# Kernel tuning notes

Hardware: AMD Instinct MI355X
Metric: run time of the kernel (lower is better)

Reference implementation:

```python
import jax, jax.numpy as jnp
import numpy as np

HEAD_NUM = 16
PAD = 0.0
MASKS_FUTURE = True


def setup_inputs() -> dict:
    key = jax.random.key(0)
    ks = jax.random.split(key, 7)
    B, S, D = 2, 2048, 1024
    scale = 0.02
    return {
        "q": jax.random.normal(ks[0], (B, S, D), dtype=jnp.float32),
        "k": jax.random.normal(ks[1], (B, S, D), dtype=jnp.float32),
        "v": jax.random.normal(ks[2], (B, S, D), dtype=jnp.float32),
        "w_q": jax.random.normal(ks[3], (D, D), dtype=jnp.float32) * scale,
        "w_k": jax.random.normal(ks[4], (D, D), dtype=jnp.float32) * scale,
        "w_v": jax.random.normal(ks[5], (D, D), dtype=jnp.float32) * scale,
        "w_o": jax.random.normal(ks[6], (D, D), dtype=jnp.float32) * scale,
    }


def _split_head(x):
    # [B, S, D] -> [B, H, S, D/H]
    B, S, D = x.shape
    return x.reshape(B, S, HEAD_NUM, D // HEAD_NUM).transpose(0, 2, 1, 3)


def reference(q, k, v, w_q, w_k, w_v, w_o):
    qp = _split_head(q @ w_q)  # [B, H, Sq, dk]
    kp = _split_head(k @ w_k)  # [B, H, Sk, dk]
    vp = _split_head(v @ w_v)  # [B, H, Sk, dv]
    d_k = qp.shape[-1]
    scores = jnp.einsum("bhqd,bhkd->bhqk", qp, kp) / jnp.sqrt(jnp.float32(d_k))
    # mask where scores equal PAD (faithful to tf.equal(head_qk, PAD))
    mask = scores == PAD
    if MASKS_FUTURE:
        # tf.linalg.band_part(mask, -1, 0): keep lower triangle, zero elsewhere
        Sq, Sk = scores.shape[-2], scores.shape[-1]
        tril = jnp.tril(jnp.ones((Sq, Sk), dtype=bool))
        mask = mask & tril
    neg = jnp.finfo(jnp.float32).min
    scores = jnp.where(mask, neg, scores)
    attn = jax.nn.softmax(scores, axis=-1)
    # keep_prob = 1.0 -> dropout is identity
    attn = jnp.where(mask, PAD, attn)
    out = jnp.einsum("bhqk,bhkd->bhqd", attn, vp)  # [B, H, Sq, dv/H]
    B, H, S, dh = out.shape
    concat = out.transpose(0, 2, 1, 3).reshape(B, S, H * dh)
    return concat @ w_o
```

## Files before the change

kernel.cpp:

```cpp
#include <hip/hip_runtime.h>
#include <hip/hip_bf16.h>

typedef unsigned short u16;
typedef unsigned int u32;
typedef short short8 __attribute__((ext_vector_type(8)));
typedef float float4v __attribute__((ext_vector_type(4)));
typedef u32 u32x2 __attribute__((ext_vector_type(2)));

#define SEQ 2048
#define DIM 1024
#define NHEAD 16
#define MROWS 4096
#define NE ((size_t)MROWS * DIM)
#define WN ((size_t)DIM * DIM)

#if __has_builtin(__builtin_amdgcn_exp2f)
#define EXP2(x) __builtin_amdgcn_exp2f(x)
#else
#define EXP2(x) exp2f(x)
#endif

__device__ inline u16 f2bf(float f) {
    union { float f; unsigned u; } v; v.f = f;
    unsigned r = v.u + 0x7fffu + ((v.u >> 16) & 1u);
    return (u16)(r >> 16);
}
__device__ inline float bf2f(u16 s) {
    union { unsigned u; float f; } v; v.u = ((unsigned)s) << 16;
    return v.f;
}
__device__ inline u32 pk2bf(float a, float b) {
    union { __hip_bfloat162 h; u32 u; } cv;
    cv.h = __float22bfloat162_rn(float2{a, b});
    return cv.u;
}
__device__ inline void gld16(const void* g, void* l) {
    __builtin_amdgcn_global_load_lds(
        (const __attribute__((address_space(1))) void*)g,
        (__attribute__((address_space(3))) void*)l, 16, 0, 0);
}

__global__ __launch_bounds__(256) void convert_qkv(
    const float* __restrict__ q, const float* __restrict__ k,
    const float* __restrict__ v, u16* __restrict__ dst)
{
    const int z = blockIdx.y;
    const float* s = (z == 0) ? q : (z == 1) ? k : v;
    const size_t i = ((size_t)blockIdx.x * 256 + threadIdx.x) * 8;
    float4v a = *(const float4v*)(s + i);
    float4v b = *(const float4v*)(s + i + 4);
    short8 o;
    for (int e = 0; e < 4; e++) { o[e] = (short)f2bf(a[e]); o[4 + e] = (short)f2bf(b[e]); }
    *(short8*)(dst + z * NE + i) = o;
}

__global__ __launch_bounds__(256) void transpose_w(
    const float* __restrict__ w0, const float* __restrict__ w1,
    const float* __restrict__ w2, const float* __restrict__ w3,
    u16* __restrict__ Wt)
{
    __shared__ u16 T[64 * 66];
    const int z = blockIdx.z;
    const float* src = (z == 0) ? w0 : (z == 1) ? w1 : (z == 2) ? w2 : w3;
    const int kt = blockIdx.x * 64, nt = blockIdx.y * 64;
    const int tid = threadIdx.x;

    {
        const int row = tid >> 2, cg = (tid & 3) * 16;
        const float* sp = src + (size_t)(kt + row) * DIM + nt + cg;
        for (int i4 = 0; i4 < 4; i4++) {
            float4v f = *(const float4v*)(sp + i4 * 4);
            for (int e = 0; e < 4; e++)
                T[row * 66 + cg + i4 * 4 + e] = f2bf(f[e]);
        }
    }
    __syncthreads();
    {
        const int nr = tid >> 2, kg = (tid & 3) * 16;
        u16* dp = Wt + (size_t)z * WN + (size_t)(nt + nr) * DIM + kt + kg;
        short8 o0, o1;
        for (int e = 0; e < 8; e++) {
            o0[e] = (short)T[(kg + e) * 66 + nr];
            o1[e] = (short)T[(kg + 8 + e) * 66 + nr];
        }
        *(short8*)(dp) = o0;
        *(short8*)(dp + 8) = o1;
    }
}

__global__ __launch_bounds__(256) void transpose_v(
    const u16* __restrict__ Vn, u16* __restrict__ Vt)
{
    __shared__ u16 T[64 * 72];
    const int bh = blockIdx.x, s0 = blockIdx.y * 64;
    const int b = bh >> 4, h = bh & 15;
    const int tid = threadIdx.x;
    for (int cc = 0; cc < 2; cc++) {
        int c = tid + cc * 256;
        const u16* src = Vn + (size_t)(b * SEQ + s0 + (c >> 3)) * DIM + h * 64 + (c & 7) * 8;
        *(short8*)&T[(c >> 3) * 72 + (c & 7) * 8] = *(const short8*)src;
    }
    __syncthreads();
    for (int cc = 0; cc < 2; cc++) {
        int c = tid + cc * 256;
        int d = c >> 3, sc_ = c & 7;
        short8 o;
        for (int e = 0; e < 8; e++) o[e] = (short)T[(sc_ * 8 + e) * 72 + d];
        *(short8*)(Vt + ((size_t)bh * 64 + d) * SEQ + s0 + sc_ * 8) = o;
    }
}

template <typename OT>
__device__ __forceinline__ void gemm_body(
    const u16* __restrict__ A, const u16* __restrict__ W, OT* __restrict__ C)
{
    __shared__ u16 Alds[128 * 32];
    __shared__ u16 Wlds[128 * 32];

    const int tid = threadIdx.x;
    const int lane = tid & 63;
    const int quad = lane >> 4, l16 = lane & 15;
    const int wave = tid >> 6, wr = wave >> 1, wc = wave & 1;
    const int m0 = blockIdx.x * 128, n0 = blockIdx.y * 128;

    float4v acc[4][4];
    float4v vz = {0.f, 0.f, 0.f, 0.f};
    for (int i = 0; i < 4; i++)
        for (int j = 0; j < 4; j++) acc[i][j] = vz;

    const int c0 = tid, c1 = 256 + tid;
    const u16* a0 = A + (size_t)(m0 + (c0 >> 2)) * DIM + (c0 & 3) * 8;
    const u16* a1 = A + (size_t)(m0 + (c1 >> 2)) * DIM + (c1 & 3) * 8;
    const u16* w0 = W + (size_t)(n0 + (c0 >> 2)) * DIM + (c0 & 3) * 8;
    const u16* w1 = W + (size_t)(n0 + (c1 >> 2)) * DIM + (c1 & 3) * 8;

    for (int k0 = 0; k0 < DIM; k0 += 32) {
        gld16(a0 + k0, &Alds[c0 * 8]);
        gld16(a1 + k0, &Alds[c1 * 8]);
        gld16(w0 + k0, &Wlds[c0 * 8]);
        gld16(w1 + k0, &Wlds[c1 * 8]);
        __syncthreads();

        short8 a[4], b[4];
        for (int i = 0; i < 4; i++)
            a[i] = *(const short8*)&Alds[(wr * 64 + i * 16 + l16) * 32 + quad * 8];
        for (int j = 0; j < 4; j++)
            b[j] = *(const short8*)&Wlds[(wc * 64 + j * 16 + l16) * 32 + quad * 8];
        for (int i = 0; i < 4; i++)
            for (int j = 0; j < 4; j++)
                acc[i][j] = __builtin_amdgcn_mfma_f32_16x16x32_bf16(a[i], b[j], acc[i][j], 0, 0, 0);
        __syncthreads();
    }

    for (int i = 0; i < 4; i++) {
        int row = m0 + wr * 64 + i * 16 + quad * 4;
        for (int j = 0; j < 4; j++) {
            int col = n0 + wc * 64 + j * 16 + l16;
            for (int r = 0; r < 4; r++) {
                if constexpr (__is_same(OT, float))
                    C[(size_t)(row + r) * DIM + col] = acc[i][j][r];
                else
                    C[(size_t)(row + r) * DIM + col] = f2bf(acc[i][j][r]);
            }
        }
    }
}

__global__ __launch_bounds__(256) void gemm_qkv(
    const u16* __restrict__ Abf, const u16* __restrict__ Wt, u16* __restrict__ QKVb)
{
    const int z = blockIdx.z;
    gemm_body<u16>(Abf + (size_t)z * NE, Wt + (size_t)(z + 1) * WN, QKVb + (size_t)z * NE);
}
__global__ __launch_bounds__(256) void gemm_out(
    const u16* __restrict__ Cb, const u16* __restrict__ Wt, float* __restrict__ out)
{
    gemm_body<float>(Cb, Wt, out);
}

__global__ __launch_bounds__(256) void attn_kernel(
    const u16* __restrict__ Q, const u16* __restrict__ K,
    const u16* __restrict__ Vtg, u16* __restrict__ O)
{
    __shared__ u16 Klds[128 * 64];
    __shared__ u16 Vt[64 * 128];
    __shared__ u16 Pl[4][64 * 40];
    __shared__ float Llds[4][64];
    float* bufA = (float*)Klds;
    float* bufB = (float*)Vt;

    const int bh = blockIdx.x;
    const int q0 = blockIdx.y * 64;
    const int tid = threadIdx.x;
    const int lane = tid & 63, w = tid >> 6;
    const int quad = lane >> 4, l16 = lane & 15;

    const size_t base = (size_t)(bh >> 4) * SEQ * DIM + (bh & 15) * 64;
    const u16* Qp = Q + base;
    const u16* Kp = K + base;
    u16* Op = O + base;
    const u16* Vp = Vtg + (size_t)bh * 64 * SEQ;

    short8 qb[4][2];
    {
        const float sc = 0.125f * 1.44269504088896f;
        for (int qc = 0; qc < 4; qc++)
            for (int s = 0; s < 2; s++) {
                short8 t = *(const short8*)(Qp + (size_t)(q0 + qc * 16 + l16) * DIM + s * 32 + quad * 8);
                for (int e = 0; e < 8; e++) t[e] = (short)f2bf(bf2f((u16)t[e]) * sc);
                qb[qc][s] = t;
            }
    }

    float4v acc[4][4];
    float4v vz = {0.f, 0.f, 0.f, 0.f};
    for (int qc = 0; qc < 4; qc++)
        for (int nb = 0; nb < 4; nb++) acc[qc][nb] = vz;
    float lp[4] = {0.f, 0.f, 0.f, 0.f};

    u16* pw = Pl[w];

    for (int kt = 0; kt < SEQ / 128; kt++) {
        const int k0 = kt * 128;
        for (int i = 0; i < 4; i++) {
            const int ck = tid + i * 256;
            const int rk = ck >> 3, sk = (ck & 7) ^ (rk & 7);
            gld16(Kp + (size_t)(k0 + rk) * DIM + sk * 8, &Klds[ck * 8]);
            const int cv = tid + i * 256;
            const int dv = cv >> 4, pv = cv & 15;
            const int sv = (pv & 8) | ((pv ^ (dv & 7)) & 7);
            gld16(Vp + (size_t)dv * SEQ + k0 + sv * 8, &Vt[cv * 8]);
        }
        __syncthreads();

        float4v st[2][4];
        for (int kr = 0; kr < 2; kr++) {
            const int row = w * 32 + kr * 16 + l16;
            short8 ka0 = *(const short8*)&Klds[row * 64 + ((quad ^ (l16 & 7)) * 8)];
            short8 ka1 = *(const short8*)&Klds[row * 64 + (((4 + quad) ^ (l16 & 7)) * 8)];
            for (int qc = 0; qc < 4; qc++) {
                float4v t = __builtin_amdgcn_mfma_f32_16x16x32_bf16(ka0, qb[qc][0], vz, 0, 0, 0);
                st[kr][qc] = __builtin_amdgcn_mfma_f32_16x16x32_bf16(ka1, qb[qc][1], t, 0, 0, 0);
            }
        }

        for (int kr = 0; kr < 2; kr++)
            for (int qc = 0; qc < 4; qc++) {
                float p0 = EXP2(st[kr][qc][0]), p1 = EXP2(st[kr][qc][1]);
                float p2 = EXP2(st[kr][qc][2]), p3 = EXP2(st[kr][qc][3]);
                lp[qc] += (p0 + p1) + (p2 + p3);
                u32x2 pk; pk[0] = pk2bf(p0, p1); pk[1] = pk2bf(p2, p3);
                *(u32x2*)((u32*)pw + (qc * 16 + l16) * 20 + kr * 8 + quad * 2) = pk;
            }
        asm volatile("" ::: "memory");

        short8 pa[4], vb[4];
        for (int qc = 0; qc < 4; qc++)
            pa[qc] = *(const short8*)&pw[(qc * 16 + l16) * 40 + quad * 8];
        for (int nb = 0; nb < 4; nb++) {
            const int gk = w * 4 + quad;
            const int pos = (gk & 8) | ((gk ^ (l16 & 7)) & 7);
            vb[nb] = *(const short8*)&Vt[(nb * 16 + l16) * 128 + pos * 8];
        }
        for (int qc = 0; qc < 4; qc++)
            for (int nb = 0; nb < 4; nb++)
                acc[qc][nb] = __builtin_amdgcn_mfma_f32_16x16x32_bf16(pa[qc], vb[nb], acc[qc][nb], 0, 0, 0);
        __syncthreads();
    }

    for (int qc = 0; qc < 4; qc++) {
        lp[qc] += __shfl_xor(lp[qc], 16);
        lp[qc] += __shfl_xor(lp[qc], 32);
    }
    if (quad == 0)
        for (int qc = 0; qc < 4; qc++) Llds[w][qc * 16 + l16] = lp[qc];

    if (w == 0 || w == 2) {
        float* buf = (w == 0) ? bufA : bufB;
        for (int qc = 0; qc < 4; qc++)
            for (int nb = 0; nb < 4; nb++)
                for (int r = 0; r < 4; r++)
                    buf[(qc * 16 + quad * 4 + r) * 64 + nb * 16 + l16] = acc[qc][nb][r];
    }
    __syncthreads();
    if (w == 1 || w == 3) {
        float* buf = (w == 1) ? bufA : bufB;
        for (int qc = 0; qc < 4; qc++)
            for (int nb = 0; nb < 4; nb++)
                for (int r = 0; r < 4; r++)
                    buf[(qc * 16 + quad * 4 + r) * 64 + nb * 16 + l16] += acc[qc][nb][r];
    }
    __syncthreads();

    {
        const int q = tid >> 2, dg = (tid & 3) * 16;
        const float l = Llds[0][q] + Llds[1][q] + Llds[2][q] + Llds[3][q];
        const float inv = 1.0f / l;
        short8 o0, o1;
        for (int e = 0; e < 8; e++) {
            o0[e] = (short)f2bf((bufA[q * 64 + dg + e] + bufB[q * 64 + dg + e]) * inv);
            o1[e] = (short)f2bf((bufA[q * 64 + dg + 8 + e] + bufB[q * 64 + dg + 8 + e]) * inv);
        }
        u16* dp = Op + (size_t)(q0 + q) * DIM + dg;
        *(short8*)(dp) = o0;
        *(short8*)(dp + 8) = o1;
    }
}

extern "C" void kernel_launch(void* const* d_in, const int* in_sizes, int n_in,
                              void* d_out, int out_size, void* d_ws, size_t ws_size,
                              hipStream_t stream)
{
    const float* q   = (const float*)d_in[0];
    const float* k   = (const float*)d_in[1];
    const float* v   = (const float*)d_in[2];
    const float* w_q = (const float*)d_in[3];
    const float* w_k = (const float*)d_in[4];
    const float* w_v = (const float*)d_in[5];
    const float* w_o = (const float*)d_in[6];
    float* out = (float*)d_out;

    u16* Abf  = (u16*)d_ws;
    u16* Wt   = Abf + 3 * NE;
    u16* QKVb = Wt + 4 * WN;
    u16* Vtg  = QKVb + 3 * NE;
    u16* Cb   = Abf;

    dim3 blk(256);
    convert_qkv<<<dim3(2048, 3), blk, 0, stream>>>(q, k, v, Abf);
    transpose_w<<<dim3(16, 16, 4), blk, 0, stream>>>(w_o, w_q, w_k, w_v, Wt);
    gemm_qkv<<<dim3(32, 8, 3), blk, 0, stream>>>(Abf, Wt, QKVb);
    transpose_v<<<dim3(32, 32), blk, 0, stream>>>(QKVb + 2 * NE, Vtg);
    attn_kernel<<<dim3(32, 32), blk, 0, stream>>>(QKVb, QKVb + NE, Vtg, Cb);
    gemm_out<<<dim3(32, 8), blk, 0, stream>>>(Cb, Wt, out);
}
```

Baseline: 247.8 us.

## Merge prep kernels, fuse V transpose into QKV GEMM, widen K-tile with swizzled LDS

Merges the input conversion and weight transpose into a single prep launch. The V transpose kernel goes away: the QKV GEMM writes V already transposed through an XOR-swizzled LDS staging buffer. Both GEMMs now use a K-tile of 64 with an XOR-swizzled LDS layout to cut bank conflicts and halve the number of barriers. The output GEMM uses 64-row tiles so more blocks fill the device. Together these remove two launches and one global round trip of V, at the cost of more LDS per block.

```diff
diff --git a/kernel.cpp b/kernel.cpp
--- a/kernel.cpp
+++ b/kernel.cpp
@@ -40,31 +40,32 @@
         (__attribute__((address_space(3))) void*)l, 16, 0, 0);
 }
 
-__global__ __launch_bounds__(256) void convert_qkv(
+__global__ __launch_bounds__(256) void prep(
     const float* __restrict__ q, const float* __restrict__ k,
-    const float* __restrict__ v, u16* __restrict__ dst)
-{
-    const int z = blockIdx.y;
-    const float* s = (z == 0) ? q : (z == 1) ? k : v;
-    const size_t i = ((size_t)blockIdx.x * 256 + threadIdx.x) * 8;
-    float4v a = *(const float4v*)(s + i);
-    float4v b = *(const float4v*)(s + i + 4);
-    short8 o;
-    for (int e = 0; e < 4; e++) { o[e] = (short)f2bf(a[e]); o[4 + e] = (short)f2bf(b[e]); }
-    *(short8*)(dst + z * NE + i) = o;
-}
-
-__global__ __launch_bounds__(256) void transpose_w(
-    const float* __restrict__ w0, const float* __restrict__ w1,
-    const float* __restrict__ w2, const float* __restrict__ w3,
-    u16* __restrict__ Wt)
+    const float* __restrict__ v, const float* __restrict__ w_q,
+    const float* __restrict__ w_k, const float* __restrict__ w_v,
+    const float* __restrict__ w_o, u16* __restrict__ Abf, u16* __restrict__ Wt)
 {
     __shared__ u16 T[64 * 66];
-    const int z = blockIdx.z;
-    const float* src = (z == 0) ? w0 : (z == 1) ? w1 : (z == 2) ? w2 : w3;
-    const int kt = blockIdx.x * 64, nt = blockIdx.y * 64;
+    const int bx = blockIdx.x;
     const int tid = threadIdx.x;
 
+    if (bx < 6144) {
+        const int z = bx >> 11, xb = bx & 2047;
+        const float* s = (z == 0) ? q : (z == 1) ? k : v;
+        const size_t i = ((size_t)xb * 256 + tid) * 8;
+        float4v a = *(const float4v*)(s + i);
+        float4v b = *(const float4v*)(s + i + 4);
+        short8 o;
+        for (int e = 0; e < 4; e++) { o[e] = (short)f2bf(a[e]); o[4 + e] = (short)f2bf(b[e]); }
+        *(short8*)(Abf + (size_t)z * NE + i) = o;
+        return;
+    }
+
+    const int t = bx - 6144;
+    const int z = t & 3, tile = t >> 2;
+    const float* src = (z == 0) ? w_o : (z == 1) ? w_q : (z == 2) ? w_k : w_v;
+    const int kt = (tile >> 4) * 64, nt = (tile & 15) * 64;
     {
         const int row = tid >> 2, cg = (tid & 3) * 16;
         const float* sp = src + (size_t)(kt + row) * DIM + nt + cg;
@@ -88,39 +89,21 @@
     }
 }
 
-__global__ __launch_bounds__(256) void transpose_v(
-    const u16* __restrict__ Vn, u16* __restrict__ Vt)
-{
-    __shared__ u16 T[64 * 72];
-    const int bh = blockIdx.x, s0 = blockIdx.y * 64;
-    const int b = bh >> 4, h = bh & 15;
+__global__ __launch_bounds__(256) void gemm_qkv(
+    const u16* __restrict__ Abf, const u16* __restrict__ Wtg, u16* __restrict__ QKVb)
+{
+    __shared__ u16 SMEM[2 * 128 * 64];
+    u16* Alds = SMEM;
+    u16* Wlds = SMEM + 128 * 64;
+
+    const int z = blockIdx.z;
+    const u16* A = Abf + (size_t)z * NE;
+    const u16* W = Wtg + (size_t)(z + 1) * WN;
+
     const int tid = threadIdx.x;
-    for (int cc = 0; cc < 2; cc++) {
-        int c = tid + cc * 256;
-        const u16* src = Vn + (size_t)(b * SEQ + s0 + (c >> 3)) * DIM + h * 64 + (c & 7) * 8;
-        *(short8*)&T[(c >> 3) * 72 + (c & 7) * 8] = *(const short8*)src;
-    }
-    __syncthreads();
-    for (int cc = 0; cc < 2; cc++) {
-        int c = tid + cc * 256;
-        int d = c >> 3, sc_ = c & 7;
-        short8 o;
-        for (int e = 0; e < 8; e++) o[e] = (short)T[(sc_ * 8 + e) * 72 + d];
-        *(short8*)(Vt + ((size_t)bh * 64 + d) * SEQ + s0 + sc_ * 8) = o;
-    }
-}
-
-template <typename OT>
-__device__ __forceinline__ void gemm_body(
-    const u16* __restrict__ A, const u16* __restrict__ W, OT* __restrict__ C)
-{
-    __shared__ u16 Alds[128 * 32];
-    __shared__ u16 Wlds[128 * 32];
-
-    const int tid = threadIdx.x;
-    const int lane = tid & 63;
+    const int lane = tid & 63, w = tid >> 6;
     const int quad = lane >> 4, l16 = lane & 15;
-    const int wave = tid >> 6, wr = wave >> 1, wc = wave & 1;
+    const int wr = w >> 1, wc = w & 1;
     const int m0 = blockIdx.x * 128, n0 = blockIdx.y * 128;
 
     float4v acc[4][4];
@@ -128,54 +111,125 @@
     for (int i = 0; i < 4; i++)
         for (int j = 0; j < 4; j++) acc[i][j] = vz;
 
-    const int c0 = tid, c1 = 256 + tid;
-    const u16* a0 = A + (size_t)(m0 + (c0 >> 2)) * DIM + (c0 & 3) * 8;
-    const u16* a1 = A + (size_t)(m0 + (c1 >> 2)) * DIM + (c1 & 3) * 8;
-    const u16* w0 = W + (size_t)(n0 + (c0 >> 2)) * DIM + (c0 & 3) * 8;
-    const u16* w1 = W + (size_t)(n0 + (c1 >> 2)) * DIM + (c1 & 3) * 8;
-
-    for (int k0 = 0; k0 < DIM; k0 += 32) {
-        gld16(a0 + k0, &Alds[c0 * 8]);
-        gld16(a1 + k0, &Alds[c1 * 8]);
-        gld16(w0 + k0, &Wlds[c0 * 8]);
-        gld16(w1 + k0, &Wlds[c1 * 8]);
-        __syncthreads();
-
-        short8 a[4], b[4];
-        for (int i = 0; i < 4; i++)
-            a[i] = *(const short8*)&Alds[(wr * 64 + i * 16 + l16) * 32 + quad * 8];
-        for (int j = 0; j < 4; j++)
-            b[j] = *(const short8*)&Wlds[(wc * 64 + j * 16 + l16) * 32 + quad * 8];
-        for (int i = 0; i < 4; i++)
-            for (int j = 0; j < 4; j++)
-                acc[i][j] = __builtin_amdgcn_mfma_f32_16x16x32_bf16(a[i], b[j], acc[i][j], 0, 0, 0);
-        __syncthreads();
-    }
-
-    for (int i = 0; i < 4; i++) {
-        int row = m0 + wr * 64 + i * 16 + quad * 4;
+    for (int k0 = 0; k0 < DIM; k0 += 64) {
+        for (int i = 0; i < 4; i++) {
+            const int c = tid + i * 256;
+            const int row = c >> 3, scc = (c & 7) ^ (row & 7);
+            gld16(A + (size_t)(m0 + row) * DIM + k0 + scc * 8, &Alds[c * 8]);
+            gld16(W + (size_t)(n0 + row) * DIM + k0 + scc * 8, &Wlds[c * 8]);
+        }
+        __syncthreads();
+
+        for (int s = 0; s < 2; s++) {
+            short8 a[4], b[4];
+            for (int i = 0; i < 4; i++) {
+                const int row = wr * 64 + i * 16 + l16;
+                a[i] = *(const short8*)&Alds[row * 64 + (((s * 4 + quad) ^ (row & 7)) * 8)];
+            }
+            for (int j = 0; j < 4; j++) {
+                const int row = wc * 64 + j * 16 + l16;
+                b[j] = *(const short8*)&Wlds[row * 64 + (((s * 4 + quad) ^ (row & 7)) * 8)];
+            }
+            for (int i = 0; i < 4; i++)
+                for (int j = 0; j < 4; j++)
+                    acc[i][j] = __builtin_amdgcn_mfma_f32_16x16x32_bf16(a[i], b[j], acc[i][j], 0, 0, 0);
+        }
+        __syncthreads();
+    }
+
+    if (z < 2) {
+        for (int i = 0; i < 4; i++) {
+            int row = m0 + wr * 64 + i * 16 + quad * 4;
+            for (int j = 0; j < 4; j++) {
+                int col = n0 + wc * 64 + j * 16 + l16;
+                for (int r = 0; r < 4; r++)
+                    QKVb[(size_t)z * NE + (size_t)(row + r) * DIM + col] = f2bf(acc[i][j][r]);
+            }
+        }
+        return;
+    }
+
+    u16* T = SMEM;
+    for (int i = 0; i < 4; i++)
+        for (int j = 0; j < 4; j++) {
+            const int d = wc * 64 + j * 16 + l16;
+            for (int r = 0; r < 4; r++) {
+                const int s = wr * 64 + i * 16 + quad * 4 + r;
+                T[d * 128 + (((s >> 3) ^ (d & 7)) * 8) + (s & 7)] = f2bf(acc[i][j][r]);
+            }
+        }
+    __syncthreads();
+    {
+        u16* Vt = QKVb + 2 * NE;
+        const int b = m0 >> 11, s_loc = m0 & 2047, h0 = n0 >> 6;
+        const int c = lane & 15;
+        for (int p = 0; p < 8; p++) {
+            const int d = w * 32 + (lane >> 4) * 8 + p;
+            short8 val = *(const short8*)&T[d * 128 + ((c ^ (d & 7)) * 8)];
+            u16* dp = Vt + ((size_t)(b * 16 + h0 + (d >> 6)) * 64 + (d & 63)) * SEQ + s_loc + c * 8;
+            *(short8*)dp = val;
+        }
+    }
+}
+
+__global__ __launch_bounds__(256) void gemm_out(
+    const u16* __restrict__ Cb, const u16* __restrict__ Wtg, float* __restrict__ out)
+{
+    __shared__ u16 Alds[64 * 64];
+    __shared__ u16 Wlds[128 * 64];
+    const u16* W = Wtg;
+
+    const int tid = threadIdx.x;
+    const int lane = tid & 63, w = tid >> 6;
+    const int quad = lane >> 4, l16 = lane & 15;
+    const int wr = w >> 1, wc = w & 1;
+    const int m0 = blockIdx.x * 64, n0 = blockIdx.y * 128;
+
+    float4v acc[2][4];
+    float4v vz = {0.f, 0.f, 0.f, 0.f};
+    for (int i = 0; i < 2; i++)
+        for (int j = 0; j < 4; j++) acc[i][j] = vz;
+
+    for (int k0 = 0; k0 < DIM; k0 += 64) {
+        {
+            for (int i = 0; i < 2; i++) {
+                const int c = tid + i * 256;
+                const int row = c >> 3, scc = (c & 7) ^ (row & 7);
+                gld16(Cb + (size_t)(m0 + row) * DIM + k0 + scc * 8, &Alds[c * 8]);
+            }
+            for (int i = 0; i < 4; i++) {
+                const int c = tid + i * 256;
+                const int row = c >> 3, scc = (c & 7) ^ (row & 7);
+                gld16(W + (size_t)(n0 + row) * DIM + k0 + scc * 8, &Wlds[c * 8]);
+            }
+        }
+        __syncthreads();
+
+        for (int s = 0; s < 2; s++) {
+            short8 a[2], b[4];
+            for (int i = 0; i < 2; i++) {
+                const int row = wr * 32 + i * 16 + l16;
+                a[i] = *(const short8*)&Alds[row * 64 + (((s * 4 + quad) ^ (row & 7)) * 8)];
+            }
+            for (int j = 0; j < 4; j++) {
+                const int row = wc * 64 + j * 16 + l16;
+                b[j] = *(const short8*)&Wlds[row * 64 + (((s * 4 + quad) ^ (row & 7)) * 8)];
+            }
+            for (int i = 0; i < 2; i++)
+                for (int j = 0; j < 4; j++)
+                    acc[i][j] = __builtin_amdgcn_mfma_f32_16x16x32_bf16(a[i], b[j], acc[i][j], 0, 0, 0);
+        }
+        __syncthreads();
+    }
+
+    for (int i = 0; i < 2; i++) {
+        int row = m0 + wr * 32 + i * 16 + quad * 4;
         for (int j = 0; j < 4; j++) {
             int col = n0 + wc * 64 + j * 16 + l16;
-            for (int r = 0; r < 4; r++) {
-                if constexpr (__is_same(OT, float))
-                    C[(size_t)(row + r) * DIM + col] = acc[i][j][r];
-                else
-                    C[(size_t)(row + r) * DIM + col] = f2bf(acc[i][j][r]);
-            }
-        }
-    }
-}
-
-__global__ __launch_bounds__(256) void gemm_qkv(
-    const u16* __restrict__ Abf, const u16* __restrict__ Wt, u16* __restrict__ QKVb)
-{
-    const int z = blockIdx.z;
-    gemm_body<u16>(Abf + (size_t)z * NE, Wt + (size_t)(z + 1) * WN, QKVb + (size_t)z * NE);
-}
-__global__ __launch_bounds__(256) void gemm_out(
-    const u16* __restrict__ Cb, const u16* __restrict__ Wt, float* __restrict__ out)
-{
-    gemm_body<float>(Cb, Wt, out);
+            for (int r = 0; r < 4; r++)
+                out[(size_t)(row + r) * DIM + col] = acc[i][j][r];
+        }
+    }
 }
 
 __global__ __launch_bounds__(256) void attn_kernel(
@@ -323,14 +377,11 @@
     u16* Abf  = (u16*)d_ws;
     u16* Wt   = Abf + 3 * NE;
     u16* QKVb = Wt + 4 * WN;
-    u16* Vtg  = QKVb + 3 * NE;
     u16* Cb   = Abf;
 
     dim3 blk(256);
-    convert_qkv<<<dim3(2048, 3), blk, 0, stream>>>(q, k, v, Abf);
-    transpose_w<<<dim3(16, 16, 4), blk, 0, stream>>>(w_o, w_q, w_k, w_v, Wt);
+    prep<<<dim3(7168), blk, 0, stream>>>(q, k, v, w_q, w_k, w_v, w_o, Abf, Wt);
     gemm_qkv<<<dim3(32, 8, 3), blk, 0, stream>>>(Abf, Wt, QKVb);
-    transpose_v<<<dim3(32, 32), blk, 0, stream>>>(QKVb + 2 * NE, Vtg);
-    attn_kernel<<<dim3(32, 32), blk, 0, stream>>>(QKVb, QKVb + NE, Vtg, Cb);
-    gemm_out<<<dim3(32, 8), blk, 0, stream>>>(Cb, Wt, out);
-}
+    attn_kernel<<<dim3(32, 32), blk, 0, stream>>>(QKVb, QKVb + NE, QKVb + 2 * NE, Cb);
+    gemm_out<<<dim3(64, 8), blk, 0, stream>>>(Cb, Wt, out);
+}
```

After: 237.3 us. -4.2%, faster.
